# Kernel tuning notes

Measured on AMD Instinct MI355X. Metric: run time of the kernel, lower is better.

The kernel has to match this reference:

```python
import jax, jax.numpy as jnp
import numpy as np

BS = 4  # gating blocksize


def setup_inputs() -> dict:
    key = jax.random.key(0)
    k1, k2, k3 = jax.random.split(key, 3)
    batch, rows, width, cols = 8, 2048, 4096, 4096
    X = jax.random.normal(k1, (batch, rows, width), dtype=jnp.float32)
    W = jax.random.normal(k2, (width, cols), dtype=jnp.float32)
    G = jax.random.normal(k3, (batch, width // BS, cols // BS), dtype=jnp.float32)
    return {"X": X, "W": W, "G": G}


def _gmm(X, W, G):
    # Y[b,r,c] = sum_k X[b,r,k] * W[k,c] * G[b, k//BS, c//BS]
    b = X.shape[0]
    # expand block gates to elementwise resolution
    Gf = jnp.repeat(jnp.repeat(G, BS, axis=1), BS, axis=2)  # (b, width, cols)
    # per-batch gated weight, then batched GEMM
    return jnp.einsum('brk,kc,bkc->brc', X, W, Gf)


def reference(X, W, G):
    Y = _gmm(X, W, G)
    s = Y.sum()
    return s * s
```

## Files before the change

### kernel.cpp

```cpp
#include <hip/hip_runtime.h>

#define BATCH 8
#define ROWS  2048
#define WIDTH 4096
#define COLS  4096
#define KB    1024
#define CBV   1024
#define ZPART 32
#define RCH   64
#define NDOT  256

typedef float f32x4 __attribute__((ext_vector_type(4)));

__global__ __launch_bounds__(256) void fused_kernel(const f32x4* __restrict__ X,
                                                    const f32x4* __restrict__ Wv,
                                                    const f32x4* __restrict__ Gv,
                                                    f32x4* __restrict__ part,
                                                    float* __restrict__ wg) {
    const int t = threadIdx.x;
    if (!(blockIdx.x & 1)) {
        const int s  = blockIdx.x >> 1;
        const int k4 = (s & 3) * 256 + t;
        const int b  = (s >> 2) & 7;
        const int z  = s >> 5;

        const f32x4* p = X + (size_t)(b * ROWS + z * RCH) * (WIDTH / 4) + k4;
        f32x4 a = {0.f, 0.f, 0.f, 0.f};
#pragma unroll 8
        for (int r = 0; r < RCH; ++r) {
            f32x4 v = p[(size_t)r * (WIDTH / 4)];
            a.x += v.x; a.y += v.y; a.z += v.z; a.w += v.w;
        }
        part[((size_t)(z * BATCH + b) << 10) + k4] = a;
    } else {
        const int kb = blockIdx.x >> 1;
        const int lane = t & 63, wv = t >> 6;

        f32x4 w[4][4];
#pragma unroll
        for (int j = 0; j < 4; ++j)
#pragma unroll
            for (int m = 0; m < 4; ++m)
                w[j][m] = Wv[(size_t)(4 * kb + j) * CBV + 4 * t + m];

        f32x4 g[8];
#pragma unroll
        for (int b = 0; b < 8; ++b)
            g[b] = Gv[((size_t)(b * KB + kb) << 8) + t];

        float w4[4][4];
#pragma unroll
        for (int j = 0; j < 4; ++j)
#pragma unroll
            for (int m = 0; m < 4; ++m)
                w4[j][m] = (w[j][m].x + w[j][m].y) + (w[j][m].z + w[j][m].w);

        float acc[8][4];
#pragma unroll
        for (int b = 0; b < 8; ++b)
#pragma unroll
            for (int j = 0; j < 4; ++j)
                acc[b][j] = g[b].x * w4[j][0] + g[b].y * w4[j][1] +
                            g[b].z * w4[j][2] + g[b].w * w4[j][3];

        __shared__ float lds[4][32];
#pragma unroll
        for (int v = 0; v < 32; ++v) {
            float x = acc[v >> 2][v & 3];
#pragma unroll
            for (int o = 1; o < 64; o <<= 1) x += __shfl_xor(x, o, 64);
            if (lane == 0) lds[wv][v] = x;
        }
        __syncthreads();
        if (t < 32) {
            float r = (lds[0][t] + lds[1][t]) + (lds[2][t] + lds[3][t]);
            wg[(size_t)(t >> 2) * WIDTH + 4 * kb + (t & 3)] = r;
        }
    }
}

__global__ __launch_bounds__(256) void dot_kernel(const f32x4* __restrict__ part,
                                                  const f32x4* __restrict__ wgv,
                                                  float* __restrict__ partial) {
    const int z  = blockIdx.x >> 3;
    const int kc = blockIdx.x & 7;
    const f32x4* pz = part + ((size_t)z * BATCH << 10);

    float acc = 0.f;
#pragma unroll
    for (int rep = 0; rep < 4; ++rep) {
        const int i = (kc << 10) + rep * 256 + threadIdx.x;
        f32x4 a = pz[i], b = wgv[i];
        acc += a.x * b.x + a.y * b.y + a.z * b.z + a.w * b.w;
    }
#pragma unroll
    for (int o = 1; o < 64; o <<= 1) acc += __shfl_xor(acc, o, 64);
    __shared__ float lds[4];
    const int lane = threadIdx.x & 63, wv = threadIdx.x >> 6;
    if (lane == 0) lds[wv] = acc;
    __syncthreads();
    if (threadIdx.x == 0) partial[blockIdx.x] = (lds[0] + lds[1]) + (lds[2] + lds[3]);
}

__global__ __launch_bounds__(256) void square_kernel(const float* __restrict__ partial,
                                                     float* __restrict__ out) {
    float v = partial[threadIdx.x];
#pragma unroll
    for (int o = 1; o < 64; o <<= 1) v += __shfl_xor(v, o, 64);
    __shared__ float lds[4];
    const int lane = threadIdx.x & 63, wv = threadIdx.x >> 6;
    if (lane == 0) lds[wv] = v;
    __syncthreads();
    if (threadIdx.x == 0) {
        float s = (lds[0] + lds[1]) + (lds[2] + lds[3]);
        out[0] = s * s;
    }
}

extern "C" void kernel_launch(void* const* d_in, const int* in_sizes, int n_in,
                              void* d_out, int out_size, void* d_ws, size_t ws_size,
                              hipStream_t stream) {
    const float* X = (const float*)d_in[0];
    const float* W = (const float*)d_in[1];
    const float* G = (const float*)d_in[2];
    float* out = (float*)d_out;

    float* part    = (float*)d_ws;
    float* wg      = part + (size_t)ZPART * BATCH * WIDTH;
    float* partial = wg + (size_t)BATCH * WIDTH;

    fused_kernel<<<2048, 256, 0, stream>>>((const f32x4*)X, (const f32x4*)W,
                                           (const f32x4*)G, (f32x4*)part, wg);

    dot_kernel<<<NDOT, 256, 0, stream>>>((const f32x4*)part, (const f32x4*)wg, partial);

    square_kernel<<<1, 256, 0, stream>>>(partial, out);
}
```

Baseline: 77.54 us.

## Merge three kernels into one persistent cooperative kernel with grid syncs

Replaces the three-kernel pipeline (column-sum/gate, dot, square) with a single cooperative persistent kernel of 512 blocks. Each block does two column-sum slices and two gate slices, alternating their order by block parity so X streaming overlaps with W/G loads, keeps the column sums in registers instead of writing partials to memory, then uses grid syncs for the dot and final square. This removes two kernel launches and the partial-buffer round trip, at the cost of grid-wide barrier overhead and lower occupancy (512 blocks). The old three-kernel path is kept as a fallback if the cooperative launch fails.

```diff
diff --git a/kernel.cpp b/kernel.cpp
--- a/kernel.cpp
+++ b/kernel.cpp
@@ -1,4 +1,7 @@
 #include <hip/hip_runtime.h>
+#include <hip/hip_cooperative_groups.h>
+
+namespace cg = cooperative_groups;
 
 #define BATCH 8
 #define ROWS  2048
@@ -11,6 +14,129 @@
 #define NDOT  256
 
 typedef float f32x4 __attribute__((ext_vector_type(4)));
+
+__device__ __forceinline__ f32x4 do_colsum(const f32x4* __restrict__ X, int s, int t) {
+    const int k4 = (s & 3) * 256 + t;
+    const int b  = (s >> 2) & 7;
+    const int z  = s >> 5;
+    const f32x4* p = X + (size_t)(b * ROWS + z * RCH) * (WIDTH / 4) + k4;
+    f32x4 a = {0.f, 0.f, 0.f, 0.f};
+#pragma unroll 8
+    for (int r = 0; r < RCH; ++r) {
+        f32x4 v = p[(size_t)r * (WIDTH / 4)];
+        a.x += v.x; a.y += v.y; a.z += v.z; a.w += v.w;
+    }
+    return a;
+}
+
+__device__ __forceinline__ void do_gate(const f32x4* __restrict__ Wv,
+                                        const f32x4* __restrict__ Gv,
+                                        float* __restrict__ wg,
+                                        float lds[4][32], int kb, int t) {
+    const int lane = t & 63, wv = t >> 6;
+
+    f32x4 g[8];
+#pragma unroll
+    for (int b = 0; b < 8; ++b)
+        g[b] = Gv[((size_t)(b * KB + kb) << 8) + t];
+
+    float w4[4][4];
+#pragma unroll
+    for (int jp = 0; jp < 2; ++jp) {
+        f32x4 wj[2][4];
+#pragma unroll
+        for (int j = 0; j < 2; ++j)
+#pragma unroll
+            for (int m = 0; m < 4; ++m)
+                wj[j][m] = Wv[(size_t)(4 * kb + 2 * jp + j) * CBV + 4 * t + m];
+#pragma unroll
+        for (int j = 0; j < 2; ++j)
+#pragma unroll
+            for (int m = 0; m < 4; ++m)
+                w4[2 * jp + j][m] = (wj[j][m].x + wj[j][m].y) + (wj[j][m].z + wj[j][m].w);
+    }
+
+    float acc[8][4];
+#pragma unroll
+    for (int b = 0; b < 8; ++b)
+#pragma unroll
+        for (int j = 0; j < 4; ++j)
+            acc[b][j] = g[b].x * w4[j][0] + g[b].y * w4[j][1] +
+                        g[b].z * w4[j][2] + g[b].w * w4[j][3];
+
+#pragma unroll
+    for (int v = 0; v < 32; ++v) {
+        float x = acc[v >> 2][v & 3];
+#pragma unroll
+        for (int o = 1; o < 64; o <<= 1) x += __shfl_xor(x, o, 64);
+        if (lane == 0) lds[wv][v] = x;
+    }
+    __syncthreads();
+    if (t < 32) {
+        float r = (lds[0][t] + lds[1][t]) + (lds[2][t] + lds[3][t]);
+        wg[(size_t)(t >> 2) * WIDTH + 4 * kb + (t & 3)] = r;
+    }
+    __syncthreads();
+}
+
+__global__ __launch_bounds__(256) void persist_kernel(const f32x4* __restrict__ X,
+                                                      const f32x4* __restrict__ Wv,
+                                                      const f32x4* __restrict__ Gv,
+                                                      float* __restrict__ wg,
+                                                      float* __restrict__ partial,
+                                                      float* __restrict__ out) {
+    const int t   = threadIdx.x;
+    const int bid = blockIdx.x;
+    const int s0  = bid, s1 = bid + 512;
+    __shared__ float lds[4][32];
+
+    f32x4 a0, a1;
+    if (bid & 1) {
+        do_gate(Wv, Gv, wg, lds, s0, t);
+        a0 = do_colsum(X, s0, t);
+        do_gate(Wv, Gv, wg, lds, s1, t);
+        a1 = do_colsum(X, s1, t);
+    } else {
+        a0 = do_colsum(X, s0, t);
+        do_gate(Wv, Gv, wg, lds, s0, t);
+        a1 = do_colsum(X, s1, t);
+        do_gate(Wv, Gv, wg, lds, s1, t);
+    }
+
+    cg::this_grid().sync();
+
+    const int lane = t & 63, wvi = t >> 6;
+#pragma unroll
+    for (int i = 0; i < 2; ++i) {
+        const int s = i ? s1 : s0;
+        const f32x4 a = i ? a1 : a0;
+        const int k4 = (s & 3) * 256 + t;
+        const int b  = (s >> 2) & 7;
+        f32x4 wv4 = ((const f32x4*)wg)[((size_t)b << 10) + k4];
+        float d = a.x * wv4.x + a.y * wv4.y + a.z * wv4.z + a.w * wv4.w;
+#pragma unroll
+        for (int o = 1; o < 64; o <<= 1) d += __shfl_xor(d, o, 64);
+        if (lane == 0) lds[wvi][i] = d;
+        __syncthreads();
+        if (t == 0) partial[s] = (lds[0][i] + lds[1][i]) + (lds[2][i] + lds[3][i]);
+        __syncthreads();
+    }
+
+    cg::this_grid().sync();
+
+    if (bid == 0) {
+        f32x4 v = ((const f32x4*)partial)[t];
+        float acc = (v.x + v.y) + (v.z + v.w);
+#pragma unroll
+        for (int o = 1; o < 64; o <<= 1) acc += __shfl_xor(acc, o, 64);
+        if (lane == 0) lds[wvi][2] = acc;
+        __syncthreads();
+        if (t == 0) {
+            float sv = (lds[0][2] + lds[1][2]) + (lds[2][2] + lds[3][2]);
+            out[0] = sv * sv;
+        }
+    }
+}
 
 __global__ __launch_bounds__(256) void fused_kernel(const f32x4* __restrict__ X,
                                                     const f32x4* __restrict__ Wv,
@@ -23,7 +149,6 @@
         const int k4 = (s & 3) * 256 + t;
         const int b  = (s >> 2) & 7;
         const int z  = s >> 5;
-
         const f32x4* p = X + (size_t)(b * ROWS + z * RCH) * (WIDTH / 4) + k4;
         f32x4 a = {0.f, 0.f, 0.f, 0.f};
 #pragma unroll 8
@@ -34,48 +159,8 @@
         part[((size_t)(z * BATCH + b) << 10) + k4] = a;
     } else {
         const int kb = blockIdx.x >> 1;
-        const int lane = t & 63, wv = t >> 6;
-
-        f32x4 w[4][4];
-#pragma unroll
-        for (int j = 0; j < 4; ++j)
-#pragma unroll
-            for (int m = 0; m < 4; ++m)
-                w[j][m] = Wv[(size_t)(4 * kb + j) * CBV + 4 * t + m];
-
-        f32x4 g[8];
-#pragma unroll
-        for (int b = 0; b < 8; ++b)
-            g[b] = Gv[((size_t)(b * KB + kb) << 8) + t];
-
-        float w4[4][4];
-#pragma unroll
-        for (int j = 0; j < 4; ++j)
-#pragma unroll
-            for (int m = 0; m < 4; ++m)
-                w4[j][m] = (w[j][m].x + w[j][m].y) + (w[j][m].z + w[j][m].w);
-
-        float acc[8][4];
-#pragma unroll
-        for (int b = 0; b < 8; ++b)
-#pragma unroll
-            for (int j = 0; j < 4; ++j)
-                acc[b][j] = g[b].x * w4[j][0] + g[b].y * w4[j][1] +
-                            g[b].z * w4[j][2] + g[b].w * w4[j][3];
-
         __shared__ float lds[4][32];
-#pragma unroll
-        for (int v = 0; v < 32; ++v) {
-            float x = acc[v >> 2][v & 3];
-#pragma unroll
-            for (int o = 1; o < 64; o <<= 1) x += __shfl_xor(x, o, 64);
-            if (lane == 0) lds[wv][v] = x;
-        }
-        __syncthreads();
-        if (t < 32) {
-            float r = (lds[0][t] + lds[1][t]) + (lds[2][t] + lds[3][t]);
-            wg[(size_t)(t >> 2) * WIDTH + 4 * kb + (t & 3)] = r;
-        }
+        do_gate(Wv, Gv, wg, lds, kb, t);
     }
 }
 
@@ -85,7 +170,6 @@
     const int z  = blockIdx.x >> 3;
     const int kc = blockIdx.x & 7;
     const f32x4* pz = part + ((size_t)z * BATCH << 10);
-
     float acc = 0.f;
 #pragma unroll
     for (int rep = 0; rep < 4; ++rep) {
@@ -103,8 +187,8 @@
 }
 
 __global__ __launch_bounds__(256) void square_kernel(const float* __restrict__ partial,
-                                                     float* __restrict__ out) {
-    float v = partial[threadIdx.x];
+                                                     int n, float* __restrict__ out) {
+    float v = (threadIdx.x < n) ? partial[threadIdx.x] : 0.f;
 #pragma unroll
     for (int o = 1; o < 64; o <<= 1) v += __shfl_xor(v, o, 64);
     __shared__ float lds[4];
@@ -120,19 +204,22 @@
 extern "C" void kernel_launch(void* const* d_in, const int* in_sizes, int n_in,
                               void* d_out, int out_size, void* d_ws, size_t ws_size,
                               hipStream_t stream) {
-    const float* X = (const float*)d_in[0];
-    const float* W = (const float*)d_in[1];
-    const float* G = (const float*)d_in[2];
+    const f32x4* X  = (const f32x4*)d_in[0];
+    const f32x4* Wv = (const f32x4*)d_in[1];
+    const f32x4* Gv = (const f32x4*)d_in[2];
     float* out = (float*)d_out;
 
     float* part    = (float*)d_ws;
     float* wg      = part + (size_t)ZPART * BATCH * WIDTH;
     float* partial = wg + (size_t)BATCH * WIDTH;
 
-    fused_kernel<<<2048, 256, 0, stream>>>((const f32x4*)X, (const f32x4*)W,
-                                           (const f32x4*)G, (f32x4*)part, wg);
-
-    dot_kernel<<<NDOT, 256, 0, stream>>>((const f32x4*)part, (const f32x4*)wg, partial);
-
-    square_kernel<<<1, 256, 0, stream>>>(partial, out);
-}
+    void* args[] = {(void*)&X, (void*)&Wv, (void*)&Gv,
+                    (void*)&wg, (void*)&partial, (void*)&out};
+    hipError_t rc = hipLaunchCooperativeKernel((const void*)persist_kernel,
+                                               dim3(512), dim3(256), args, 0, stream);
+    if (rc != hipSuccess) {
+        fused_kernel<<<2048, 256, 0, stream>>>(X, Wv, Gv, (f32x4*)part, wg);
+        dot_kernel<<<NDOT, 256, 0, stream>>>((const f32x4*)part, (const f32x4*)wg, partial);
+        square_kernel<<<1, 256, 0, stream>>>(partial, 256, out);
+    }
+}
```

Result: slower. 203.5 us (+162.4%).
